# Performance work log

Measured on AMD Instinct MI355X. Metric: run time of the kernel, lower is better.

## Reference

```python
import jax, jax.numpy as jnp
import numpy as np

NUM_SPECIAL = 3  # rows 1..NUM_SPECIAL in special table; row 0 is padding (zeros)

def setup_inputs() -> dict:
    key = jax.random.key(0)
    ks = jax.random.split(key, 16)
    T, B, E, H, L, V = 128, 32, 512, 512, 2, 32000
    G = 4 * H
    s = 0.02
    special_emb = jax.random.normal(ks[1], (NUM_SPECIAL + 1, E), jnp.float32) * s
    special_emb = special_emb.at[0].set(0.0)  # padding_idx=0
    return {
        "ids": jax.random.randint(ks[0], (T, B), 0, V),
        "length_countdown": jax.random.uniform(ks[2], (T, B, 1), jnp.float32),
        "word_emb": jax.random.normal(ks[3], (V, E), jnp.float32) * s,
        "special_emb": special_emb,
        "h0": jax.random.normal(ks[4], (L, B, H), jnp.float32) * s,
        "c0": jax.random.normal(ks[5], (L, B, H), jnp.float32) * s,
        "prev_output": jnp.zeros((B, H), jnp.float32),
        "Wih0": jax.random.normal(ks[6], (G, E + H + 1), jnp.float32) * s,
        "Whh0": jax.random.normal(ks[7], (G, H), jnp.float32) * s,
        "bih0": jnp.zeros((G,), jnp.float32),
        "bhh0": jnp.zeros((G,), jnp.float32),
        "Wih1": jax.random.normal(ks[8], (G, H), jnp.float32) * s,
        "Whh1": jax.random.normal(ks[9], (G, H), jnp.float32) * s,
        "bih1": jnp.zeros((G,), jnp.float32),
        "bhh1": jnp.zeros((G,), jnp.float32),
        "Wg": jax.random.normal(ks[10], (V, H), jnp.float32) * s,
        "bg": jnp.zeros((V,), jnp.float32),
    }

def _lstm_cell(x, h, c, Wih, Whh, bih, bhh):
    gates = x @ Wih.T + bih + h @ Whh.T + bhh  # [B, 4H]
    i, f, g, o = jnp.split(gates, 4, axis=-1)  # torch LSTMCell gate order
    c_new = jax.nn.sigmoid(f) * c + jax.nn.sigmoid(i) * jnp.tanh(g)
    h_new = jax.nn.sigmoid(o) * jnp.tanh(c_new)
    return h_new, c_new

def reference(ids, length_countdown, word_emb, special_emb, h0, c0, prev_output,
              Wih0, Whh0, bih0, bhh0, Wih1, Whh1, bih1, bhh1, Wg, bg):
    # embeddings = word_embeddings(ids) + special_embeddings(special_ids(ids))
    sp_ids = jnp.where(ids < NUM_SPECIAL, ids + 1, 0)
    emb = word_emb[ids] + special_emb[sp_ids]                 # [T,B,E]
    rnn_in = jnp.concatenate([emb, length_countdown], axis=2)  # [T,B,E+1]

    Wihs = (Wih0, Wih1); Whhs = (Whh0, Whh1)
    bihs = (bih0, bih1); bhhs = (bhh0, bhh1)
    L = h0.shape[0]

    def step(carry, emb_t):
        out, h, c = carry
        x = jnp.concatenate([emb_t, out], axis=1)  # input feeding
        hs, cs = [], []
        for l in range(L):
            h_l, c_l = _lstm_cell(x, h[l], c[l], Wihs[l], Whhs[l], bihs[l], bhhs[l])
            x = h_l  # dropout=0
            hs.append(h_l); cs.append(c_l)
        out = x
        score = jax.nn.log_softmax(out @ Wg.T + bg, axis=-1)  # generator
        return (out, jnp.stack(hs), jnp.stack(cs)), score

    (out, hT, cT), scores = jax.lax.scan(step, (prev_output, h0, c0), rnn_in)
    return scores, (hT, cT), out
```

## Files before the change

kernel.cpp:

```cpp
#include <hip/hip_runtime.h>
#include <hip/hip_bf16.h>


typedef __attribute__((ext_vector_type(8))) short bf16x8;
typedef __attribute__((ext_vector_type(4))) float f32x4;
typedef __attribute__((ext_vector_type(2))) unsigned long long u64x2;

#define AS1 __attribute__((address_space(1)))
#define AS3 __attribute__((address_space(3)))

__device__ __forceinline__ unsigned short f2bf(float f) {
  unsigned int u = __builtin_bit_cast(unsigned int, f);
  u += 0x7fffu + ((u >> 16) & 1u);
  return (unsigned short)(u >> 16);
}

__device__ __forceinline__ void gl16(const void* g, void* l) {
  __builtin_amdgcn_global_load_lds((const AS1 unsigned int*)g,
                                   (AS3 unsigned int*)l, 16, 0, 0);
}

__device__ __forceinline__ float sigm(float x) { return 1.0f / (1.0f + __expf(-x)); }

__global__ __launch_bounds__(256, 1) void prep_k(
    const float* __restrict__ Wg,  const float* __restrict__ Wih0,
    const float* __restrict__ Whh0,const float* __restrict__ Wih1,
    const float* __restrict__ Whh1,const float* __restrict__ bih0,
    const float* __restrict__ bhh0,const float* __restrict__ bih1,
    const float* __restrict__ bhh1,const float* __restrict__ h0,
    const float* __restrict__ pout,
    unsigned short* __restrict__ WgBf, unsigned short* __restrict__ W0e,
    unsigned short* __restrict__ Wr0p, unsigned short* __restrict__ Wr1p,
    float* __restrict__ b1p, float* __restrict__ bias0c,
    float* __restrict__ wcd, unsigned short* __restrict__ H0X,
    unsigned short* __restrict__ FOUT, unsigned short* __restrict__ H1I)
{
  const long N0 = 16384000L;
  const long N1 = N0 + 1048576L;
  const long N2 = N1 + 2097152L;
  const long N3 = N2 + 2097152L;
  const long N4 = N3 + 2048L;
  const long N5 = N4 + 2048L;
  const long N6 = N5 + 2048L;
  const long N7 = N6 + 49152L;
  for (long i = blockIdx.x * 256L + threadIdx.x; i < N7; i += 256L * gridDim.x) {
    if (i < N0) {
      WgBf[i] = f2bf(Wg[i]);
    } else if (i < N1) {
      long k = i - N0; int g = (int)(k >> 9); int kk = (int)(k & 511);
      W0e[k] = f2bf(Wih0[g * 1025 + kk]);
    } else if (i < N2) {
      long k = i - N1; int gp = (int)(k >> 10); int kk = (int)(k & 1023);
      int j = gp >> 2, gate = gp & 3; int g = gate * 512 + j;
      float v = (kk < 512) ? Whh0[g * 512 + kk] : Wih0[g * 1025 + 513 + (kk - 512)];
      Wr0p[k] = f2bf(v);
    } else if (i < N3) {
      long k = i - N2; int gp = (int)(k >> 10); int kk = (int)(k & 1023);
      int j = gp >> 2, gate = gp & 3; int g = gate * 512 + j;
      float v = (kk < 512) ? Wih1[g * 512 + kk] : Whh1[g * 512 + (kk - 512)];
      Wr1p[k] = f2bf(v);
    } else if (i < N4) {
      int gp = (int)(i - N3); int j = gp >> 2, gate = gp & 3; int g = gate * 512 + j;
      b1p[gp] = bih1[g] + bhh1[g];
    } else if (i < N5) {
      int g = (int)(i - N4); bias0c[g] = bih0[g] + bhh0[g];
    } else if (i < N6) {
      int g = (int)(i - N5); wcd[g] = Wih0[g * 1025 + 512];
    } else {
      long k = i - N6;
      int sub = (int)(k >> 14);
      int e = (int)(k & 16383);
      int wgx = e >> 9, b = (e >> 4) & 31, jl = e & 15;
      int j = wgx * 16 + jl;
      float v = (sub == 0) ? h0[b * 512 + j]
              : (sub == 1) ? h0[16384 + b * 512 + j]
                           : pout[b * 512 + j];
      unsigned short* dst = (sub == 0) ? H0X : (sub == 1) ? H1I : FOUT;
      dst[e] = f2bf(v);
    }
  }
}

__global__ __launch_bounds__(256, 1) void emb_k(
    const int* __restrict__ ids, const float* __restrict__ wemb,
    const float* __restrict__ semb, unsigned short* __restrict__ ebf)
{
  const int tb = blockIdx.x;
  const int id = ids[tb];
  const int sp = (id < 3) ? (id + 1) : 0;
  const float* wr = wemb + (long)id * 512;
  const float* sr = semb + sp * 512;
  for (int i = threadIdx.x; i < 512; i += 256)
    ebf[tb * 512 + i] = f2bf(wr[i] + sr[i]);
}

template<int EPI>
__global__ __launch_bounds__(256, 1) void gemm_bt(
    const unsigned short* __restrict__ A,
    const unsigned short* __restrict__ B, int N,
    float* __restrict__ C,
    const float* __restrict__ e0, const float* __restrict__ e1,
    const float* __restrict__ e2)
{
  __shared__ unsigned short sA[4096];
  __shared__ unsigned short sB[4096];
  const int tid = threadIdx.x;
  const int l = tid & 63, w = tid >> 6;
  const int nb = N >> 7;
  const int bid = blockIdx.x;
  const int bm = bid / nb, bn = bid - bm * nb;

  const int u0 = w * 128 + l;
  const int u1 = u0 + 64;
  const int r0 = u0 >> 2, c0 = (u0 & 3) ^ (r0 & 3);
  const int r1 = u1 >> 2, c1 = (u1 & 3) ^ (r1 & 3);
  const unsigned short* ga0 = A + (long)(bm * 128 + r0) * 512 + c0 * 8;
  const unsigned short* ga1 = A + (long)(bm * 128 + r1) * 512 + c1 * 8;
  const unsigned short* gb0 = B + (long)(bn * 128 + r0) * 512 + c0 * 8;
  const unsigned short* gb1 = B + (long)(bn * 128 + r1) * 512 + c1 * 8;
  unsigned short* la0 = sA + (w * 2 + 0) * 512;
  unsigned short* la1 = sA + (w * 2 + 1) * 512;
  unsigned short* lb0 = sB + (w * 2 + 0) * 512;
  unsigned short* lb1 = sB + (w * 2 + 1) * 512;

  const int fr = l & 15, fc = l >> 4;
  const int wm = w >> 1, wn = w & 1;
  int aoff[4], boff[4];
#pragma unroll
  for (int mi = 0; mi < 4; ++mi) {
    int row = wm * 64 + mi * 16 + fr;
    aoff[mi] = row * 64 + ((fc ^ (row & 3)) * 16);
  }
#pragma unroll
  for (int ni = 0; ni < 4; ++ni) {
    int row = wn * 64 + ni * 16 + fr;
    boff[ni] = row * 64 + ((fc ^ (row & 3)) * 16);
  }

  f32x4 acc[4][4];
#pragma unroll
  for (int i = 0; i < 4; ++i)
#pragma unroll
    for (int jq = 0; jq < 4; ++jq) acc[i][jq] = (f32x4){0.f, 0.f, 0.f, 0.f};

  for (int kt = 0; kt < 16; ++kt) {
    __syncthreads();
    gl16(ga0 + kt * 32, la0);
    gl16(ga1 + kt * 32, la1);
    gl16(gb0 + kt * 32, lb0);
    gl16(gb1 + kt * 32, lb1);
    asm volatile("s_waitcnt vmcnt(0)" ::: "memory");
    __syncthreads();
    bf16x8 av[4], bv[4];
#pragma unroll
    for (int mi = 0; mi < 4; ++mi)
      av[mi] = *(const bf16x8*)((const char*)sA + aoff[mi]);
#pragma unroll
    for (int ni = 0; ni < 4; ++ni)
      bv[ni] = *(const bf16x8*)((const char*)sB + boff[ni]);
#pragma unroll
    for (int mi = 0; mi < 4; ++mi)
#pragma unroll
      for (int ni = 0; ni < 4; ++ni)
        acc[mi][ni] = __builtin_amdgcn_mfma_f32_16x16x32_bf16(av[mi], bv[ni], acc[mi][ni], 0, 0, 0);
  }

  const int mbase = bm * 128 + wm * 64;
  const int nbase = bn * 128 + wn * 64;
#pragma unroll
  for (int mi = 0; mi < 4; ++mi)
#pragma unroll
    for (int ni = 0; ni < 4; ++ni) {
      const int col = nbase + ni * 16 + fr;
#pragma unroll
      for (int r = 0; r < 4; ++r) {
        const int row = mbase + mi * 16 + fc * 4 + r;
        float v = acc[mi][ni][r];
        if (EPI == 0) {
          const int gp = ((row & 511) << 2) | (row >> 9);
          v += e0[row] + e2[col] * e1[row];
          C[(long)gp * N + col] = v;
        } else {
          v += e0[col];
          C[(long)row * N + col] = v;
        }
      }
    }
}

__global__ __launch_bounds__(256, 1) void lstm_seq(
    const unsigned short* __restrict__ Wr0p,
    const unsigned short* __restrict__ Wr1p,
    const float* __restrict__ P0t, const float* __restrict__ b1p,
    const float* __restrict__ c0in,
    unsigned short* __restrict__ H0X, unsigned short* __restrict__ H1X,
    const unsigned short* __restrict__ FOUT, const unsigned short* __restrict__ H1I,
    unsigned short* __restrict__ outbf, float* __restrict__ outs,
    unsigned int* __restrict__ flagA, unsigned int* __restrict__ flagB)
{
  const int tid = threadIdx.x;
  const int wg = blockIdx.x;
  const int l = tid & 63, w = tid >> 6;
  const int fr = l & 15, fc = l >> 4;

  __shared__ unsigned short sx[32768];
  __shared__ float sg[32][65];
  __shared__ unsigned short sh[32][16];

  const int b = tid & 31, jl0 = tid >> 5;
  const int sb = l >> 1, sjh = l & 1;

  float c0r[2], c1r[2], h0k[2], h1k[2];
#pragma unroll
  for (int jq = 0; jq < 2; ++jq) {
    c0r[jq] = c0in[b * 512 + wg * 16 + jl0 + jq * 8];
    c1r[jq] = c0in[16384 + b * 512 + wg * 16 + jl0 + jq * 8];
    h0k[jq] = 0.f; h1k[jq] = 0.f;
  }

  float b1v[8];
#pragma unroll
  for (int jq = 0; jq < 2; ++jq)
#pragma unroll
    for (int g = 0; g < 4; ++g)
      b1v[jq * 4 + g] = b1p[(wg * 16 + jl0 + jq * 8) * 4 + g];

  const char* sxb0 = (const char*)sx + fr * 2048;
  const char* sxb1 = (const char*)sx + (16 + fr) * 2048;
  const int xr = (fr & 7) << 4;
  const int wrow = (wg * 64 + w * 16 + fr) * 1024 + fc * 8;

  char* const sxw = (char*)sx + sb * 2048;
  const int sswz = (sb & 7) << 4;

#define STAGE2(srcp, half)                                                    \
  do {                                                                        \
    unsigned long long q0[8], q1[8];                                          \
    _Pragma("unroll")                                                         \
    for (int i = 0; i < 8; ++i) {                                             \
      int u = i * 256 + tid;                                                  \
      q0[i] = __hip_atomic_load((const unsigned long long*)(srcp) + u * 2,    \
                                __ATOMIC_RELAXED, __HIP_MEMORY_SCOPE_AGENT);  \
      q1[i] = __hip_atomic_load((const unsigned long long*)(srcp) + u * 2 + 1,\
                                __ATOMIC_RELAXED, __HIP_MEMORY_SCOPE_AGENT);  \
    }                                                                         \
    _Pragma("unroll")                                                         \
    for (int i = 0; i < 8; ++i) {                                             \
      int cb = (half) * 1024 + (i * 4 + w) * 32 + sjh * 16;                   \
      u64x2 v; v.x = q0[i]; v.y = q1[i];                                      \
      *(u64x2*)(sxw + (cb ^ sswz)) = v;                                       \
    }                                                                         \
  } while (0)

#define MFMA_HALF(Wp, k0, a0v, a1v)                                           \
  do {                                                                        \
    _Pragma("unroll")                                                         \
    for (int kt = (k0); kt < (k0) + 16; ++kt) {                               \
      bf16x8 bv = *(const bf16x8*)((Wp) + wrow + kt * 32);                    \
      bf16x8 x0 = *(const bf16x8*)(sxb0 + ((kt * 64 + fc * 16) ^ xr));        \
      bf16x8 x1 = *(const bf16x8*)(sxb1 + ((kt * 64 + fc * 16) ^ xr));        \
      a0v = __builtin_amdgcn_mfma_f32_16x16x32_bf16(x0, bv, a0v, 0, 0, 0);    \
      a1v = __builtin_amdgcn_mfma_f32_16x16x32_bf16(x1, bv, a1v, 0, 0, 0);    \
    }                                                                         \
  } while (0)

#define POLL(flags, tgt)                                                      \
  do {                                                                        \
    const unsigned int* fp = (flags) + ((l & 31) << 5);                       \
    for (;;) {                                                                \
      unsigned int f = __hip_atomic_load(fp, __ATOMIC_RELAXED,                \
                                         __HIP_MEMORY_SCOPE_AGENT);           \
      if (__all((int)(f >= (unsigned int)(tgt)))) break;                      \
      __builtin_amdgcn_s_sleep(1);                                            \
    }                                                                         \
    asm volatile("" ::: "memory");                                            \
  } while (0)

  STAGE2(H0X, 0);
  __syncthreads();
  if (tid == 0)
    __hip_atomic_store(&flagB[wg << 5], 1u, __ATOMIC_RELAXED, __HIP_MEMORY_SCOPE_AGENT);

  for (int t = 0; t < 128; ++t) {
    float p0v[8];
#pragma unroll
    for (int jq = 0; jq < 2; ++jq)
#pragma unroll
      for (int g = 0; g < 4; ++g)
        p0v[jq * 4 + g] =
            P0t[(long)((wg * 16 + jl0 + jq * 8) * 4 + g) * 4096 + t * 32 + b];

    f32x4 accA0 = (f32x4){0.f, 0.f, 0.f, 0.f};
    f32x4 accA1 = (f32x4){0.f, 0.f, 0.f, 0.f};
    MFMA_HALF(Wr0p, 0, accA0, accA1);

    POLL(flagB, t + 1);
    if (t == 0) STAGE2(FOUT, 1); else STAGE2(H1X, 1);
    __syncthreads();
    MFMA_HALF(Wr0p, 16, accA0, accA1);
#pragma unroll
    for (int r = 0; r < 4; ++r) {
      sg[fc * 4 + r][w * 16 + fr] = accA0[r];
      sg[16 + fc * 4 + r][w * 16 + fr] = accA1[r];
    }
    __syncthreads();
#pragma unroll
    for (int jq = 0; jq < 2; ++jq) {
      const int jl = jl0 + jq * 8;
      float gi = sg[b][jl * 4 + 0] + p0v[jq * 4 + 0];
      float gf = sg[b][jl * 4 + 1] + p0v[jq * 4 + 1];
      float gg = sg[b][jl * 4 + 2] + p0v[jq * 4 + 2];
      float go = sg[b][jl * 4 + 3] + p0v[jq * 4 + 3];
      float cn = sigm(gf) * c0r[jq] + sigm(gi) * tanhf(gg);
      float hn = sigm(go) * tanhf(cn);
      c0r[jq] = cn; h0k[jq] = hn;
      sh[b][jl] = f2bf(hn);
    }
    __syncthreads();
    if (w == 0) {
      u64x2 v = *(const u64x2*)&sh[sb][sjh * 8];
      unsigned long long* dst =
          (unsigned long long*)(H0X + wg * 512 + sb * 16 + sjh * 8);
      __hip_atomic_store(dst,     v.x, __ATOMIC_RELAXED, __HIP_MEMORY_SCOPE_AGENT);
      __hip_atomic_store(dst + 1, v.y, __ATOMIC_RELAXED, __HIP_MEMORY_SCOPE_AGENT);
      asm volatile("s_waitcnt vmcnt(0)" ::: "memory");
      if (tid == 0)
        __hip_atomic_store(&flagA[wg << 5], (unsigned int)(t + 1),
                           __ATOMIC_RELAXED, __HIP_MEMORY_SCOPE_AGENT);
    }

    f32x4 accB0 = (f32x4){0.f, 0.f, 0.f, 0.f};
    f32x4 accB1 = (f32x4){0.f, 0.f, 0.f, 0.f};
    if (t == 0) {
      STAGE2(H1I, 1);
      __syncthreads();
    }
    MFMA_HALF(Wr1p, 16, accB0, accB1);

    POLL(flagA, t + 1);
    STAGE2(H0X, 0);
    __syncthreads();
    MFMA_HALF(Wr1p, 0, accB0, accB1);
#pragma unroll
    for (int r = 0; r < 4; ++r) {
      sg[fc * 4 + r][w * 16 + fr] = accB0[r];
      sg[16 + fc * 4 + r][w * 16 + fr] = accB1[r];
    }
    __syncthreads();
#pragma unroll
    for (int jq = 0; jq < 2; ++jq) {
      const int jl = jl0 + jq * 8;
      float gi = sg[b][jl * 4 + 0] + b1v[jq * 4 + 0];
      float gf = sg[b][jl * 4 + 1] + b1v[jq * 4 + 1];
      float gg = sg[b][jl * 4 + 2] + b1v[jq * 4 + 2];
      float go = sg[b][jl * 4 + 3] + b1v[jq * 4 + 3];
      float cn = sigm(gf) * c1r[jq] + sigm(gi) * tanhf(gg);
      float hn = sigm(go) * tanhf(cn);
      c1r[jq] = cn; h1k[jq] = hn;
      sh[b][jl] = f2bf(hn);
    }
    __syncthreads();
    if (w == 0) {
      u64x2 v = *(const u64x2*)&sh[sb][sjh * 8];
      unsigned long long* dst =
          (unsigned long long*)(H1X + wg * 512 + sb * 16 + sjh * 8);
      __hip_atomic_store(dst,     v.x, __ATOMIC_RELAXED, __HIP_MEMORY_SCOPE_AGENT);
      __hip_atomic_store(dst + 1, v.y, __ATOMIC_RELAXED, __HIP_MEMORY_SCOPE_AGENT);
      asm volatile("s_waitcnt vmcnt(0)" ::: "memory");
      if (tid == 0)
        __hip_atomic_store(&flagB[wg << 5], (unsigned int)(t + 2),
                           __ATOMIC_RELAXED, __HIP_MEMORY_SCOPE_AGENT);
    } else if (w == 1) {
      u64x2 v = *(const u64x2*)&sh[sb][sjh * 8];
      *(u64x2*)(outbf + (t * 32 + sb) * 512 + wg * 16 + sjh * 8) = v;
    }
  }
#undef STAGE2
#undef MFMA_HALF
#undef POLL

  float* hT = outs + 131072000;
  float* cT = outs + 131072000 + 32768;
  float* oT = outs + 131072000 + 65536;
#pragma unroll
  for (int jq = 0; jq < 2; ++jq) {
    const int j = wg * 16 + jl0 + jq * 8;
    hT[b * 512 + j] = h0k[jq];
    hT[16384 + b * 512 + j] = h1k[jq];
    cT[b * 512 + j] = c0r[jq];
    cT[16384 + b * 512 + j] = c1r[jq];
    oT[b * 512 + j] = h1k[jq];
  }
}

__global__ __launch_bounds__(256, 1) void lse_fix(float* __restrict__ sc)
{
  const long row = blockIdx.x;
  float4* p4 = (float4*)(sc + row * 32000L);
  const int tid = threadIdx.x;
  float m = -3.0e38f, s = 0.0f;
  for (int i = tid; i < 8000; i += 256) {
    float4 v = p4[i];
    float m4 = fmaxf(fmaxf(v.x, v.y), fmaxf(v.z, v.w));
    float mn = fmaxf(m, m4);
    s = s * __expf(m - mn) + __expf(v.x - mn) + __expf(v.y - mn)
        + __expf(v.z - mn) + __expf(v.w - mn);
    m = mn;
  }
#pragma unroll
  for (int off = 32; off > 0; off >>= 1) {
    float mo = __shfl_down(m, off);
    float so = __shfl_down(s, off);
    float mn = fmaxf(m, mo);
    s = s * __expf(m - mn) + so * __expf(mo - mn);
    m = mn;
  }
  __shared__ float lm[4], ls[4], lse_sh;
  if ((tid & 63) == 0) { lm[tid >> 6] = m; ls[tid >> 6] = s; }
  __syncthreads();
  if (tid == 0) {
    float M = lm[0], S = ls[0];
#pragma unroll
    for (int i = 1; i < 4; ++i) {
      float mn = fmaxf(M, lm[i]);
      S = S * __expf(M - mn) + ls[i] * __expf(lm[i] - mn);
      M = mn;
    }
    lse_sh = M + __logf(S);
  }
  __syncthreads();
  const float lse = lse_sh;
  for (int i = tid; i < 8000; i += 256) {
    float4 v = p4[i];
    v.x -= lse; v.y -= lse; v.z -= lse; v.w -= lse;
    p4[i] = v;
  }
}

extern "C" void kernel_launch(void* const* d_in, const int* in_sizes, int n_in,
                              void* d_out, int out_size, void* d_ws, size_t ws_size,
                              hipStream_t stream) {
  const int*   ids  = (const int*)d_in[0];
  const float* cd   = (const float*)d_in[1];
  const float* wemb = (const float*)d_in[2];
  const float* semb = (const float*)d_in[3];
  const float* h0   = (const float*)d_in[4];
  const float* c0   = (const float*)d_in[5];
  const float* pout = (const float*)d_in[6];
  const float* Wih0 = (const float*)d_in[7];
  const float* Whh0 = (const float*)d_in[8];
  const float* bih0 = (const float*)d_in[9];
  const float* bhh0 = (const float*)d_in[10];
  const float* Wih1 = (const float*)d_in[11];
  const float* Whh1 = (const float*)d_in[12];
  const float* bih1 = (const float*)d_in[13];
  const float* bhh1 = (const float*)d_in[14];
  const float* Wg   = (const float*)d_in[15];
  const float* bg   = (const float*)d_in[16];
  float* out = (float*)d_out;

  char* ws = (char*)d_ws;
  unsigned short* WgBf   = (unsigned short*)(ws);
  unsigned short* W0e    = (unsigned short*)(ws + 32768000);
  unsigned short* Wr0p   = (unsigned short*)(ws + 34865152);
  unsigned short* Wr1p   = (unsigned short*)(ws + 39059456);
  float*          b1p    = (float*)(ws + 43253760);
  float*          bias0c = (float*)(ws + 43261952);
  float*          wcd    = (float*)(ws + 43270144);
  unsigned short* embbf  = (unsigned short*)(ws + 43409408);
  unsigned short* outbf  = (unsigned short*)(ws + 47603712);
  float*          P0t    = (float*)(ws + 51798016);
  unsigned int*   flagA  = (unsigned int*)(ws + 85352448);
  unsigned int*   flagB  = (unsigned int*)(ws + 85356544);
  unsigned short* H0X    = (unsigned short*)(ws + 85360640);
  unsigned short* H1X    = (unsigned short*)(ws + 85393408);
  unsigned short* FOUT   = (unsigned short*)(ws + 85426176);
  unsigned short* H1I    = (unsigned short*)(ws + 85458944);

  hipMemsetAsync((void*)flagA, 0, 8192, stream);

  prep_k<<<8192, 256, 0, stream>>>(Wg, Wih0, Whh0, Wih1, Whh1,
                                   bih0, bhh0, bih1, bhh1, h0, pout,
                                   WgBf, W0e, Wr0p, Wr1p, b1p, bias0c, wcd,
                                   H0X, FOUT, H1I);

  emb_k<<<4096, 256, 0, stream>>>(ids, wemb, semb, embbf);

  gemm_bt<0><<<512, 256, 0, stream>>>(W0e, embbf, 4096, P0t, bias0c, wcd, cd);

  lstm_seq<<<32, 256, 0, stream>>>(Wr0p, Wr1p, P0t, b1p, c0,
                                   H0X, H1X, FOUT, H1I, outbf, out, flagA, flagB);

  gemm_bt<1><<<8000, 256, 0, stream>>>(outbf, WgBf, 32000, out, bg, nullptr, nullptr);

  lse_fix<<<4096, 256, 0, stream>>>(out);
}
```

Before: 1.956 ms.

## Replicate hidden-state exchange buffers and flags per XCC, split MFMA accumulators

The persistent LSTM kernel now writes each hidden-state slice and its ready flag into eight replicas, one per XCC. Each workgroup reads its XCC's copy (chosen via the HW_REG_XCC_ID register), so polling and staging loads can hit a closer cache instead of crossing dies. The cost is eight times as many stores and flag writes per step, plus larger workspace buffers. The MFMA loop is also split into even and odd accumulator chains, summed at the end, to shorten the dependency chain between back-to-back MFMAs.

New measurement: 1.968 ms. No clear change (+0.6%).

```diff
diff --git a/kernel.cpp b/kernel.cpp
--- a/kernel.cpp
+++ b/kernel.cpp
@@ -42,7 +42,7 @@
   const long N4 = N3 + 2048L;
   const long N5 = N4 + 2048L;
   const long N6 = N5 + 2048L;
-  const long N7 = N6 + 49152L;
+  const long N7 = N6 + 393216L;
   for (long i = blockIdx.x * 256L + threadIdx.x; i < N7; i += 256L * gridDim.x) {
     if (i < N0) {
       WgBf[i] = f2bf(Wg[i]);
@@ -68,9 +68,10 @@
       int g = (int)(i - N5); wcd[g] = Wih0[g * 1025 + 512];
     } else {
       long k = i - N6;
-      int sub = (int)(k >> 14);
-      int e = (int)(k & 16383);
-      int wgx = e >> 9, b = (e >> 4) & 31, jl = e & 15;
+      int sub = (int)(k / 131072L);
+      int e = (int)(k - (long)sub * 131072L);
+      int e2 = e & 16383;
+      int wgx = e2 >> 9, b = (e2 >> 4) & 31, jl = e2 & 15;
       int j = wgx * 16 + jl;
       float v = (sub == 0) ? h0[b * 512 + j]
               : (sub == 1) ? h0[16384 + b * 512 + j]
@@ -207,6 +208,11 @@
   __shared__ float sg[32][65];
   __shared__ unsigned short sh[32][16];
 
+  unsigned int xcc;
+  asm("s_getreg_b32 %0, hwreg(HW_REG_XCC_ID)" : "=s"(xcc));
+  const int eoff = (int)(xcc & 7) << 14;
+  const int foff = (int)(xcc & 7) << 10;
+
   const int b = tid & 31, jl0 = tid >> 5;
   const int sb = l >> 1, sjh = l & 1;
 
@@ -239,9 +245,9 @@
     _Pragma("unroll")                                                         \
     for (int i = 0; i < 8; ++i) {                                             \
       int u = i * 256 + tid;                                                  \
-      q0[i] = __hip_atomic_load((const unsigned long long*)(srcp) + u * 2,    \
+      q0[i] = __hip_atomic_load((const unsigned long long*)((srcp) + eoff) + u * 2, \
                                 __ATOMIC_RELAXED, __HIP_MEMORY_SCOPE_AGENT);  \
-      q1[i] = __hip_atomic_load((const unsigned long long*)(srcp) + u * 2 + 1,\
+      q1[i] = __hip_atomic_load((const unsigned long long*)((srcp) + eoff) + u * 2 + 1, \
                                 __ATOMIC_RELAXED, __HIP_MEMORY_SCOPE_AGENT);  \
     }                                                                         \
     _Pragma("unroll")                                                         \
@@ -252,21 +258,27 @@
     }                                                                         \
   } while (0)
 
-#define MFMA_HALF(Wp, k0, a0v, a1v)                                           \
+#define MFMA_HALF(Wp, k0, e0v, o0v, e1v, o1v)                                 \
   do {                                                                        \
     _Pragma("unroll")                                                         \
-    for (int kt = (k0); kt < (k0) + 16; ++kt) {                               \
-      bf16x8 bv = *(const bf16x8*)((Wp) + wrow + kt * 32);                    \
-      bf16x8 x0 = *(const bf16x8*)(sxb0 + ((kt * 64 + fc * 16) ^ xr));        \
-      bf16x8 x1 = *(const bf16x8*)(sxb1 + ((kt * 64 + fc * 16) ^ xr));        \
-      a0v = __builtin_amdgcn_mfma_f32_16x16x32_bf16(x0, bv, a0v, 0, 0, 0);    \
-      a1v = __builtin_amdgcn_mfma_f32_16x16x32_bf16(x1, bv, a1v, 0, 0, 0);    \
+    for (int kp = 0; kp < 8; ++kp) {                                          \
+      int kta = (k0) + kp * 2, ktb = kta + 1;                                 \
+      bf16x8 bva = *(const bf16x8*)((Wp) + wrow + kta * 32);                  \
+      bf16x8 x0a = *(const bf16x8*)(sxb0 + ((kta * 64 + fc * 16) ^ xr));      \
+      bf16x8 x1a = *(const bf16x8*)(sxb1 + ((kta * 64 + fc * 16) ^ xr));      \
+      e0v = __builtin_amdgcn_mfma_f32_16x16x32_bf16(x0a, bva, e0v, 0, 0, 0);  \
+      e1v = __builtin_amdgcn_mfma_f32_16x16x32_bf16(x1a, bva, e1v, 0, 0, 0);  \
+      bf16x8 bvb = *(const bf16x8*)((Wp) + wrow + ktb * 32);                  \
+      bf16x8 x0b = *(const bf16x8*)(sxb0 + ((ktb * 64 + fc * 16) ^ xr));      \
+      bf16x8 x1b = *(const bf16x8*)(sxb1 + ((ktb * 64 + fc * 16) ^ xr));      \
+      o0v = __builtin_amdgcn_mfma_f32_16x16x32_bf16(x0b, bvb, o0v, 0, 0, 0);  \
+      o1v = __builtin_amdgcn_mfma_f32_16x16x32_bf16(x1b, bvb, o1v, 0, 0, 0);  \
     }                                                                         \
   } while (0)
 
 #define POLL(flags, tgt)                                                      \
   do {                                                                        \
-    const unsigned int* fp = (flags) + ((l & 31) << 5);                       \
+    const unsigned int* fp = (flags) + foff + ((l & 31) << 5);                \
     for (;;) {                                                                \
       unsigned int f = __hip_atomic_load(fp, __ATOMIC_RELAXED,                \
                                          __HIP_MEMORY_SCOPE_AGENT);           \
@@ -278,8 +290,9 @@
 
   STAGE2(H0X, 0);
   __syncthreads();
-  if (tid == 0)
-    __hip_atomic_store(&flagB[wg << 5], 1u, __ATOMIC_RELAXED, __HIP_MEMORY_SCOPE_AGENT);
+  if (w == 0 && l < 8)
+    __hip_atomic_store(&flagB[l * 1024 + (wg << 5)], 1u,
+                       __ATOMIC_RELAXED, __HIP_MEMORY_SCOPE_AGENT);
 
   for (int t = 0; t < 128; ++t) {
     float p0v[8];
@@ -290,18 +303,21 @@
         p0v[jq * 4 + g] =
             P0t[(long)((wg * 16 + jl0 + jq * 8) * 4 + g) * 4096 + t * 32 + b];
 
-    f32x4 accA0 = (f32x4){0.f, 0.f, 0.f, 0.f};
-    f32x4 accA1 = (f32x4){0.f, 0.f, 0.f, 0.f};
-    MFMA_HALF(Wr0p, 0, accA0, accA1);
+    f32x4 aA0e = (f32x4){0.f,0.f,0.f,0.f}, aA0o = (f32x4){0.f,0.f,0.f,0.f};
+    f32x4 aA1e = (f32x4){0.f,0.f,0.f,0.f}, aA1o = (f32x4){0.f,0.f,0.f,0.f};
+    MFMA_HALF(Wr0p, 0, aA0e, aA0o, aA1e, aA1o);
 
     POLL(flagB, t + 1);
     if (t == 0) STAGE2(FOUT, 1); else STAGE2(H1X, 1);
     __syncthreads();
-    MFMA_HALF(Wr0p, 16, accA0, accA1);
-#pragma unroll
-    for (int r = 0; r < 4; ++r) {
-      sg[fc * 4 + r][w * 16 + fr] = accA0[r];
-      sg[16 + fc * 4 + r][w * 16 + fr] = accA1[r];
+    MFMA_HALF(Wr0p, 16, aA0e, aA0o, aA1e, aA1o);
+    {
+      f32x4 s0 = aA0e + aA0o, s1 = aA1e + aA1o;
+#pragma unroll
+      for (int r = 0; r < 4; ++r) {
+        sg[fc * 4 + r][w * 16 + fr] = s0[r];
+        sg[16 + fc * 4 + r][w * 16 + fr] = s1[r];
+      }
     }
     __syncthreads();
 #pragma unroll
@@ -319,32 +335,38 @@
     __syncthreads();
     if (w == 0) {
       u64x2 v = *(const u64x2*)&sh[sb][sjh * 8];
-      unsigned long long* dst =
+      unsigned long long* dst0 =
           (unsigned long long*)(H0X + wg * 512 + sb * 16 + sjh * 8);
-      __hip_atomic_store(dst,     v.x, __ATOMIC_RELAXED, __HIP_MEMORY_SCOPE_AGENT);
-      __hip_atomic_store(dst + 1, v.y, __ATOMIC_RELAXED, __HIP_MEMORY_SCOPE_AGENT);
+#pragma unroll
+      for (int r = 0; r < 8; ++r) {
+        __hip_atomic_store(dst0 + r * 2048,     v.x, __ATOMIC_RELAXED, __HIP_MEMORY_SCOPE_AGENT);
+        __hip_atomic_store(dst0 + r * 2048 + 1, v.y, __ATOMIC_RELAXED, __HIP_MEMORY_SCOPE_AGENT);
+      }
       asm volatile("s_waitcnt vmcnt(0)" ::: "memory");
-      if (tid == 0)
-        __hip_atomic_store(&flagA[wg << 5], (unsigned int)(t + 1),
+      if (l < 8)
+        __hip_atomic_store(&flagA[l * 1024 + (wg << 5)], (unsigned int)(t + 1),
                            __ATOMIC_RELAXED, __HIP_MEMORY_SCOPE_AGENT);
     }
 
-    f32x4 accB0 = (f32x4){0.f, 0.f, 0.f, 0.f};
-    f32x4 accB1 = (f32x4){0.f, 0.f, 0.f, 0.f};
+    f32x4 aB0e = (f32x4){0.f,0.f,0.f,0.f}, aB0o = (f32x4){0.f,0.f,0.f,0.f};
+    f32x4 aB1e = (f32x4){0.f,0.f,0.f,0.f}, aB1o = (f32x4){0.f,0.f,0.f,0.f};
     if (t == 0) {
       STAGE2(H1I, 1);
       __syncthreads();
     }
-    MFMA_HALF(Wr1p, 16, accB0, accB1);
+    MFMA_HALF(Wr1p, 16, aB0e, aB0o, aB1e, aB1o);
 
     POLL(flagA, t + 1);
     STAGE2(H0X, 0);
     __syncthreads();
-    MFMA_HALF(Wr1p, 0, accB0, accB1);
-#pragma unroll
-    for (int r = 0; r < 4; ++r) {
-      sg[fc * 4 + r][w * 16 + fr] = accB0[r];
-      sg[16 + fc * 4 + r][w * 16 + fr] = accB1[r];
+    MFMA_HALF(Wr1p, 0, aB0e, aB0o, aB1e, aB1o);
+    {
+      f32x4 s0 = aB0e + aB0o, s1 = aB1e + aB1o;
+#pragma unroll
+      for (int r = 0; r < 4; ++r) {
+        sg[fc * 4 + r][w * 16 + fr] = s0[r];
+        sg[16 + fc * 4 + r][w * 16 + fr] = s1[r];
+      }
     }
     __syncthreads();
 #pragma unroll
@@ -362,13 +384,16 @@
     __syncthreads();
     if (w == 0) {
       u64x2 v = *(const u64x2*)&sh[sb][sjh * 8];
-      unsigned long long* dst =
+      unsigned long long* dst0 =
           (unsigned long long*)(H1X + wg * 512 + sb * 16 + sjh * 8);
-      __hip_atomic_store(dst,     v.x, __ATOMIC_RELAXED, __HIP_MEMORY_SCOPE_AGENT);
-      __hip_atomic_store(dst + 1, v.y, __ATOMIC_RELAXED, __HIP_MEMORY_SCOPE_AGENT);
+#pragma unroll
+      for (int r = 0; r < 8; ++r) {
+        __hip_atomic_store(dst0 + r * 2048,     v.x, __ATOMIC_RELAXED, __HIP_MEMORY_SCOPE_AGENT);
+        __hip_atomic_store(dst0 + r * 2048 + 1, v.y, __ATOMIC_RELAXED, __HIP_MEMORY_SCOPE_AGENT);
+      }
       asm volatile("s_waitcnt vmcnt(0)" ::: "memory");
-      if (tid == 0)
-        __hip_atomic_store(&flagB[wg << 5], (unsigned int)(t + 2),
+      if (l < 8)
+        __hip_atomic_store(&flagB[l * 1024 + (wg << 5)], (unsigned int)(t + 2),
                            __ATOMIC_RELAXED, __HIP_MEMORY_SCOPE_AGENT);
     } else if (w == 1) {
       u64x2 v = *(const u64x2*)&sh[sb][sjh * 8];
@@ -471,13 +496,13 @@
   unsigned short* outbf  = (unsigned short*)(ws + 47603712);
   float*          P0t    = (float*)(ws + 51798016);
   unsigned int*   flagA  = (unsigned int*)(ws + 85352448);
-  unsigned int*   flagB  = (unsigned int*)(ws + 85356544);
-  unsigned short* H0X    = (unsigned short*)(ws + 85360640);
-  unsigned short* H1X    = (unsigned short*)(ws + 85393408);
-  unsigned short* FOUT   = (unsigned short*)(ws + 85426176);
-  unsigned short* H1I    = (unsigned short*)(ws + 85458944);
-
-  hipMemsetAsync((void*)flagA, 0, 8192, stream);
+  unsigned int*   flagB  = (unsigned int*)(ws + 85385216);
+  unsigned short* H0X    = (unsigned short*)(ws + 85417984);
+  unsigned short* H1X    = (unsigned short*)(ws + 85680128);
+  unsigned short* FOUT   = (unsigned short*)(ws + 85942272);
+  unsigned short* H1I    = (unsigned short*)(ws + 86204416);
+
+  hipMemsetAsync((void*)flagA, 0, 65536, stream);
 
   prep_k<<<8192, 256, 0, stream>>>(Wg, Wih0, Whh0, Wih1, Whh1,
                                    bih0, bhh0, bih1, bhh1, h0, pout,
```

## Fuse per-tile log-softmax max/sum partials into generator GEMM epilogue

Applied to the files above, without the earlier changes.

The generator GEMM epilogue now computes per-row max and sum-of-exp over each 128-column tile. It combines the two wave halves through shared memory and writes (max, sum) partials to a workspace buffer aliased onto the P0t region, which is no longer needed by then. lse_fix then reduces 250 partials per row instead of re-reading the full 32000-wide score row, removing one full read pass over the score matrix. The cost is extra exp, shuffle and sync work in the GEMM epilogue plus a reshuffled workspace layout.

Measured after the change: 1.911 ms. 2.3% less time.

```diff
diff --git a/kernel.cpp b/kernel.cpp
--- a/kernel.cpp
+++ b/kernel.cpp
@@ -8,6 +8,8 @@
 
 #define AS1 __attribute__((address_space(1)))
 #define AS3 __attribute__((address_space(3)))
+#define RLX __ATOMIC_RELAXED
+#define AGT __HIP_MEMORY_SCOPE_AGENT
 
 __device__ __forceinline__ unsigned short f2bf(float f) {
   unsigned int u = __builtin_bit_cast(unsigned int, f);
@@ -99,11 +101,12 @@
     const unsigned short* __restrict__ A,
     const unsigned short* __restrict__ B, int N,
     float* __restrict__ C,
-    const float* __restrict__ e0, const float* __restrict__ e1,
+    const float* __restrict__ e0, float* __restrict__ e1,
     const float* __restrict__ e2)
 {
   __shared__ unsigned short sA[4096];
   __shared__ unsigned short sB[4096];
+  __shared__ float pmw[128][2][2];
   const int tid = threadIdx.x;
   const int l = tid & 63, w = tid >> 6;
   const int nb = N >> 7;
@@ -167,25 +170,83 @@
 
   const int mbase = bm * 128 + wm * 64;
   const int nbase = bn * 128 + wn * 64;
-#pragma unroll
-  for (int mi = 0; mi < 4; ++mi)
-#pragma unroll
-    for (int ni = 0; ni < 4; ++ni) {
-      const int col = nbase + ni * 16 + fr;
-#pragma unroll
-      for (int r = 0; r < 4; ++r) {
-        const int row = mbase + mi * 16 + fc * 4 + r;
-        float v = acc[mi][ni][r];
-        if (EPI == 0) {
+
+  if (EPI == 0) {
+#pragma unroll
+    for (int mi = 0; mi < 4; ++mi)
+#pragma unroll
+      for (int ni = 0; ni < 4; ++ni) {
+        const int col = nbase + ni * 16 + fr;
+#pragma unroll
+        for (int r = 0; r < 4; ++r) {
+          const int row = mbase + mi * 16 + fc * 4 + r;
           const int gp = ((row & 511) << 2) | (row >> 9);
-          v += e0[row] + e2[col] * e1[row];
+          float v = acc[mi][ni][r] + e0[row] + e2[col] * e1[row];
           C[(long)gp * N + col] = v;
-        } else {
-          v += e0[col];
-          C[(long)row * N + col] = v;
         }
       }
-    }
+  } else {
+    float m2[4][4], s2[4][4];
+#pragma unroll
+    for (int mi = 0; mi < 4; ++mi)
+#pragma unroll
+      for (int r = 0; r < 4; ++r) { m2[mi][r] = -3.0e38f; s2[mi][r] = 0.f; }
+#pragma unroll
+    for (int mi = 0; mi < 4; ++mi)
+#pragma unroll
+      for (int ni = 0; ni < 4; ++ni) {
+        const int col = nbase + ni * 16 + fr;
+        const float bgc = e0[col];
+#pragma unroll
+        for (int r = 0; r < 4; ++r) {
+          float v = acc[mi][ni][r] + bgc;
+          acc[mi][ni][r] = v;
+          C[(long)(mbase + mi * 16 + fc * 4 + r) * N + col] = v;
+          m2[mi][r] = fmaxf(m2[mi][r], v);
+        }
+      }
+#pragma unroll
+    for (int mi = 0; mi < 4; ++mi)
+#pragma unroll
+      for (int r = 0; r < 4; ++r)
+#pragma unroll
+        for (int s = 1; s < 16; s <<= 1)
+          m2[mi][r] = fmaxf(m2[mi][r], __shfl_xor(m2[mi][r], s));
+#pragma unroll
+    for (int mi = 0; mi < 4; ++mi)
+#pragma unroll
+      for (int ni = 0; ni < 4; ++ni)
+#pragma unroll
+        for (int r = 0; r < 4; ++r)
+          s2[mi][r] += __expf(acc[mi][ni][r] - m2[mi][r]);
+#pragma unroll
+    for (int mi = 0; mi < 4; ++mi)
+#pragma unroll
+      for (int r = 0; r < 4; ++r)
+#pragma unroll
+        for (int s = 1; s < 16; s <<= 1)
+          s2[mi][r] += __shfl_xor(s2[mi][r], s);
+    if (fr == 0) {
+#pragma unroll
+      for (int mi = 0; mi < 4; ++mi)
+#pragma unroll
+        for (int r = 0; r < 4; ++r) {
+          const int rl = wm * 64 + mi * 16 + fc * 4 + r;
+          pmw[rl][wn][0] = m2[mi][r];
+          pmw[rl][wn][1] = s2[mi][r];
+        }
+    }
+    __syncthreads();
+    if (tid < 128) {
+      float ma = pmw[tid][0][0], sa = pmw[tid][0][1];
+      float mb = pmw[tid][1][0], sb = pmw[tid][1][1];
+      float M = fmaxf(ma, mb);
+      float S = sa * __expf(ma - M) + sb * __expf(mb - M);
+      float2* PMS = (float2*)e1;
+      float2 o; o.x = M; o.y = S;
+      PMS[(long)(bm * 128 + tid) * nb + bn] = o;
+    }
+  }
 }
 
 __global__ __launch_bounds__(256, 1) void lstm_seq(
@@ -240,9 +301,9 @@
     for (int i = 0; i < 8; ++i) {                                             \
       int u = i * 256 + tid;                                                  \
       q0[i] = __hip_atomic_load((const unsigned long long*)(srcp) + u * 2,    \
-                                __ATOMIC_RELAXED, __HIP_MEMORY_SCOPE_AGENT);  \
+                                RLX, AGT);                                    \
       q1[i] = __hip_atomic_load((const unsigned long long*)(srcp) + u * 2 + 1,\
-                                __ATOMIC_RELAXED, __HIP_MEMORY_SCOPE_AGENT);  \
+                                RLX, AGT);                                    \
     }                                                                         \
     _Pragma("unroll")                                                         \
     for (int i = 0; i < 8; ++i) {                                             \
@@ -268,8 +329,7 @@
   do {                                                                        \
     const unsigned int* fp = (flags) + ((l & 31) << 5);                       \
     for (;;) {                                                                \
-      unsigned int f = __hip_atomic_load(fp, __ATOMIC_RELAXED,                \
-                                         __HIP_MEMORY_SCOPE_AGENT);           \
+      unsigned int f = __hip_atomic_load(fp, RLX, AGT);                       \
       if (__all((int)(f >= (unsigned int)(tgt)))) break;                      \
       __builtin_amdgcn_s_sleep(1);                                            \
     }                                                                         \
@@ -279,7 +339,7 @@
   STAGE2(H0X, 0);
   __syncthreads();
   if (tid == 0)
-    __hip_atomic_store(&flagB[wg << 5], 1u, __ATOMIC_RELAXED, __HIP_MEMORY_SCOPE_AGENT);
+    __hip_atomic_store(&flagB[wg << 5], 1u, RLX, AGT);
 
   for (int t = 0; t < 128; ++t) {
     float p0v[8];
@@ -321,12 +381,11 @@
       u64x2 v = *(const u64x2*)&sh[sb][sjh * 8];
       unsigned long long* dst =
           (unsigned long long*)(H0X + wg * 512 + sb * 16 + sjh * 8);
-      __hip_atomic_store(dst,     v.x, __ATOMIC_RELAXED, __HIP_MEMORY_SCOPE_AGENT);
-      __hip_atomic_store(dst + 1, v.y, __ATOMIC_RELAXED, __HIP_MEMORY_SCOPE_AGENT);
+      __hip_atomic_store(dst,     v.x, RLX, AGT);
+      __hip_atomic_store(dst + 1, v.y, RLX, AGT);
       asm volatile("s_waitcnt vmcnt(0)" ::: "memory");
       if (tid == 0)
-        __hip_atomic_store(&flagA[wg << 5], (unsigned int)(t + 1),
-                           __ATOMIC_RELAXED, __HIP_MEMORY_SCOPE_AGENT);
+        __hip_atomic_store(&flagA[wg << 5], (unsigned int)(t + 1), RLX, AGT);
     }
 
     f32x4 accB0 = (f32x4){0.f, 0.f, 0.f, 0.f};
@@ -364,12 +423,11 @@
       u64x2 v = *(const u64x2*)&sh[sb][sjh * 8];
       unsigned long long* dst =
           (unsigned long long*)(H1X + wg * 512 + sb * 16 + sjh * 8);
-      __hip_atomic_store(dst,     v.x, __ATOMIC_RELAXED, __HIP_MEMORY_SCOPE_AGENT);
-      __hip_atomic_store(dst + 1, v.y, __ATOMIC_RELAXED, __HIP_MEMORY_SCOPE_AGENT);
+      __hip_atomic_store(dst,     v.x, RLX, AGT);
+      __hip_atomic_store(dst + 1, v.y, RLX, AGT);
       asm volatile("s_waitcnt vmcnt(0)" ::: "memory");
       if (tid == 0)
-        __hip_atomic_store(&flagB[wg << 5], (unsigned int)(t + 2),
-                           __ATOMIC_RELAXED, __HIP_MEMORY_SCOPE_AGENT);
+        __hip_atomic_store(&flagB[wg << 5], (unsigned int)(t + 2), RLX, AGT);
     } else if (w == 1) {
       u64x2 v = *(const u64x2*)&sh[sb][sjh * 8];
       *(u64x2*)(outbf + (t * 32 + sb) * 512 + wg * 16 + sjh * 8) = v;
@@ -393,19 +451,16 @@
   }
 }
 
-__global__ __launch_bounds__(256, 1) void lse_fix(float* __restrict__ sc)
+__global__ __launch_bounds__(256, 1) void lse_fix(float* __restrict__ sc,
+                                                  const float2* __restrict__ pms)
 {
   const long row = blockIdx.x;
   float4* p4 = (float4*)(sc + row * 32000L);
   const int tid = threadIdx.x;
   float m = -3.0e38f, s = 0.0f;
-  for (int i = tid; i < 8000; i += 256) {
-    float4 v = p4[i];
-    float m4 = fmaxf(fmaxf(v.x, v.y), fmaxf(v.z, v.w));
-    float mn = fmaxf(m, m4);
-    s = s * __expf(m - mn) + __expf(v.x - mn) + __expf(v.y - mn)
-        + __expf(v.z - mn) + __expf(v.w - mn);
-    m = mn;
+  if (tid < 250) {
+    float2 p = pms[row * 250 + tid];
+    m = p.x; s = p.y;
   }
 #pragma unroll
   for (int off = 32; off > 0; off >>= 1) {
@@ -467,15 +522,16 @@
   float*          b1p    = (float*)(ws + 43253760);
   float*          bias0c = (float*)(ws + 43261952);
   float*          wcd    = (float*)(ws + 43270144);
-  unsigned short* embbf  = (unsigned short*)(ws + 43409408);
-  unsigned short* outbf  = (unsigned short*)(ws + 47603712);
-  float*          P0t    = (float*)(ws + 51798016);
-  unsigned int*   flagA  = (unsigned int*)(ws + 85352448);
-  unsigned int*   flagB  = (unsigned int*)(ws + 85356544);
-  unsigned short* H0X    = (unsigned short*)(ws + 85360640);
-  unsigned short* H1X    = (unsigned short*)(ws + 85393408);
-  unsigned short* FOUT   = (unsigned short*)(ws + 85426176);
-  unsigned short* H1I    = (unsigned short*)(ws + 85458944);
+  unsigned short* embbf  = (unsigned short*)(ws + 43278336);
+  unsigned short* outbf  = (unsigned short*)(ws + 47472640);
+  float*          P0t    = (float*)(ws + 51666944);
+  float*          PMS    = (float*)(ws + 51666944);
+  unsigned int*   flagA  = (unsigned int*)(ws + 85221376);
+  unsigned int*   flagB  = (unsigned int*)(ws + 85225472);
+  unsigned short* H0X    = (unsigned short*)(ws + 85229568);
+  unsigned short* H1X    = (unsigned short*)(ws + 85262336);
+  unsigned short* FOUT   = (unsigned short*)(ws + 85295104);
+  unsigned short* H1I    = (unsigned short*)(ws + 85327872);
 
   hipMemsetAsync((void*)flagA, 0, 8192, stream);
 
@@ -491,7 +547,7 @@
   lstm_seq<<<32, 256, 0, stream>>>(Wr0p, Wr1p, P0t, b1p, c0,
                                    H0X, H1X, FOUT, H1I, outbf, out, flagA, flagB);
 
-  gemm_bt<1><<<8000, 256, 0, stream>>>(outbf, WgBf, 32000, out, bg, nullptr, nullptr);
-
-  lse_fix<<<4096, 256, 0, stream>>>(out);
-}
+  gemm_bt<1><<<8000, 256, 0, stream>>>(outbf, WgBf, 32000, out, bg, PMS, nullptr);
+
+  lse_fix<<<4096, 256, 0, stream>>>(out, (const float2*)PMS);
+}
```
